# Kernel optimization log

Hardware: AMD Instinct MI355X
Metric: run time of the kernel (lower is better)

## Reference

```python
import jax, jax.numpy as jnp
import numpy as np

B, L, H, NH = 4, 200, 256, 4
HS = H // NH
NEG = jnp.float32(-(2.0**32) + 1.0)


def setup_inputs() -> dict:
    key = jax.random.key(0)
    ks = jax.random.split(key, 12)
    f = lambda k, s, sc=1.0: jax.random.normal(k, s, dtype=jnp.float32) * sc
    w_sc = 1.0 / np.sqrt(H).astype(np.float32)
    return {
        "queries": f(ks[0], (B, L, H)),
        "keys": f(ks[1], (B, L, H)),
        "time_matrix_K": f(ks[2], (B, L, L, H)),
        "time_matrix_V": f(ks[3], (B, L, L, H)),
        "dis_matrix_K": f(ks[4], (B, L, L, H)),
        "dis_matrix_V": f(ks[5], (B, L, L, H)),
        "abs_pos_K": f(ks[6], (B, L, H)),
        "abs_pos_V": f(ks[7], (B, L, H)),
        "Qw": f(ks[8], (H, H), w_sc),
        "Qb": jnp.zeros((H,), jnp.float32),
        "Kw": f(ks[9], (H, H), w_sc),
        "Kb": jnp.zeros((H,), jnp.float32),
        "Vw": f(ks[10], (H, H), w_sc),
        "Vb": jnp.zeros((H,), jnp.float32),
        "time_mask": jnp.zeros((B, L), dtype=bool),          # no padding positions
        "attn_mask": ~jnp.tril(jnp.ones((L, L), dtype=bool)),  # causal: mask strict upper triangle
    }


def reference(queries, keys, time_matrix_K, time_matrix_V, dis_matrix_K, dis_matrix_V,
              abs_pos_K, abs_pos_V, Qw, Qb, Kw, Kb, Vw, Vb, time_mask, attn_mask):
    # Linear projections (torch nn.Linear: x @ W^T + b)
    Q = queries @ Qw.T + Qb
    K = keys @ Kw.T + Kb
    V = keys @ Vw.T + Vb
    # split heads: [B, L, NH, HS]
    qh = Q.reshape(B, L, NH, HS)
    kh = K.reshape(B, L, NH, HS)
    vh = V.reshape(B, L, NH, HS)
    pKh = abs_pos_K.reshape(B, L, NH, HS)
    pVh = abs_pos_V.reshape(B, L, NH, HS)
    tKh = time_matrix_K.reshape(B, L, L, NH, HS)
    tVh = time_matrix_V.reshape(B, L, L, NH, HS)
    dKh = dis_matrix_K.reshape(B, L, L, NH, HS)
    dVh = dis_matrix_V.reshape(B, L, L, NH, HS)

    # attention logits [B, NH, L(query), L(key)] with three extra bias terms
    w = jnp.einsum("blhd,bmhd->bhlm", qh, kh)
    w += jnp.einsum("blhd,bmhd->bhlm", qh, pKh)
    w += jnp.einsum("blmhd,blhd->bhlm", tKh, qh)
    w += jnp.einsum("blmhd,blhd->bhlm", dKh, qh)
    w = w / jnp.sqrt(jnp.float32(HS))

    mask = time_mask[:, None, :, None] | attn_mask[None, None, :, :]
    w = jnp.where(mask, NEG, w)
    a = jax.nn.softmax(w, axis=-1)  # dropout_rate = 0 (eval)

    out = jnp.einsum("bhlm,bmhd->blhd", a, vh)
    out += jnp.einsum("bhlm,bmhd->blhd", a, pVh)
    out += jnp.einsum("bhlm,blmhd->blhd", a, tVh)
    out += jnp.einsum("bhlm,blmhd->blhd", a, dVh)
    return out.reshape(B, L, H)
```

## Files before the change

kernel.cpp:

```cpp
#include <hip/hip_runtime.h>
#include <cstddef>


#define B 4
#define L 200
#define H 256
#define NH 4
#define HS 64
#define SCALE 0.125f
#define NROWS 4

__global__ __launch_bounds__(256) void depoi_proj(
    const float* __restrict__ queries, const float* __restrict__ keys,
    const float* __restrict__ Qw, const float* __restrict__ Qb,
    const float* __restrict__ Kw, const float* __restrict__ Kb,
    const float* __restrict__ Vw, const float* __restrict__ Vb,
    const float* __restrict__ apK, const float* __restrict__ apV,
    float* __restrict__ Qo, float* __restrict__ Ko, float* __restrict__ Vo)
{
    __shared__ float4 xq[NROWS][H / 4];
    __shared__ float4 xk[NROWS][H / 4];
    const int t  = threadIdx.x;
    const int n0 = blockIdx.x * NROWS;

    const float4* q4 = (const float4*)queries;
    const float4* k4 = (const float4*)keys;
    {
        int r = t >> 6, c = t & 63;
        xq[r][c] = q4[(size_t)(n0 + r) * (H / 4) + c];
        xk[r][c] = k4[(size_t)(n0 + r) * (H / 4) + c];
    }
    __syncthreads();

    float accq[NROWS], acck[NROWS], accv[NROWS];
#pragma unroll
    for (int r = 0; r < NROWS; ++r) { accq[r] = 0.f; acck[r] = 0.f; accv[r] = 0.f; }

    const float4* Qw4 = (const float4*)Qw + (size_t)t * (H / 4);
    const float4* Kw4 = (const float4*)Kw + (size_t)t * (H / 4);
    const float4* Vw4 = (const float4*)Vw + (size_t)t * (H / 4);
    for (int i = 0; i < H / 4; ++i) {
        float4 wq = Qw4[i], wk = Kw4[i], wv = Vw4[i];
#pragma unroll
        for (int r = 0; r < NROWS; ++r) {
            float4 a = xq[r][i];
            float4 c = xk[r][i];
            accq[r] += a.x * wq.x + a.y * wq.y + a.z * wq.z + a.w * wq.w;
            acck[r] += c.x * wk.x + c.y * wk.y + c.z * wk.z + c.w * wk.w;
            accv[r] += c.x * wv.x + c.y * wv.y + c.z * wv.z + c.w * wv.w;
        }
    }

    const float bq = Qb[t], bk = Kb[t], bv = Vb[t];
#pragma unroll
    for (int r = 0; r < NROWS; ++r) {
        size_t o = (size_t)(n0 + r) * H + t;
        Qo[o] = accq[r] + bq;
        Ko[o] = acck[r] + bk + apK[o];
        Vo[o] = accv[r] + bv + apV[o];
    }
}

__global__ __launch_bounds__(512) void depoi_attn(
    const float* __restrict__ Q, const float* __restrict__ Ksum,
    const float* __restrict__ Vsum,
    const float* __restrict__ tK, const float* __restrict__ dK,
    const float* __restrict__ tV, const float* __restrict__ dV,
    float* __restrict__ out)
{
    const int l = L - 1 - blockIdx.x;
    const int b = blockIdx.y;
    const int t    = threadIdx.x;
    const int c    = t & 63;
    const int mg   = t >> 6;
    const int lane = t & 63;
    const int hh   = c >> 4;
    const int M    = l + 1;

    __shared__ float plog[NH][208];
    __shared__ float sredA[8];
    __shared__ float sredB[8];
    __shared__ float4 wpart[8][64];

    const float4* Q4 = (const float4*)Q;
    const float4 q4  = Q4[(size_t)(b * L + l) * 64 + c];

    const float4* K4 = (const float4*)Ksum + (size_t)b * L * 64;
    const float4* T4 = (const float4*)tK + (size_t)(b * L + l) * L * 64;
    const float4* D4 = (const float4*)dK + (size_t)(b * L + l) * L * 64;

    int m = mg;
    for (; m + 8 < M; m += 16) {
        float4 k0 = K4[(size_t)m * 64 + c];
        float4 t0 = T4[(size_t)m * 64 + c];
        float4 d0 = D4[(size_t)m * 64 + c];
        float4 k1 = K4[(size_t)(m + 8) * 64 + c];
        float4 t1 = T4[(size_t)(m + 8) * 64 + c];
        float4 d1 = D4[(size_t)(m + 8) * 64 + c];
        float p0 = q4.x * (k0.x + t0.x + d0.x) + q4.y * (k0.y + t0.y + d0.y)
                 + q4.z * (k0.z + t0.z + d0.z) + q4.w * (k0.w + t0.w + d0.w);
        float p1 = q4.x * (k1.x + t1.x + d1.x) + q4.y * (k1.y + t1.y + d1.y)
                 + q4.z * (k1.z + t1.z + d1.z) + q4.w * (k1.w + t1.w + d1.w);
        p0 += __shfl_xor(p0, 1); p1 += __shfl_xor(p1, 1);
        p0 += __shfl_xor(p0, 2); p1 += __shfl_xor(p1, 2);
        p0 += __shfl_xor(p0, 4); p1 += __shfl_xor(p1, 4);
        p0 += __shfl_xor(p0, 8); p1 += __shfl_xor(p1, 8);
        if ((c & 15) == 0) {
            plog[hh][m]     = p0 * SCALE;
            plog[hh][m + 8] = p1 * SCALE;
        }
    }
    if (m < M) {
        float4 k0 = K4[(size_t)m * 64 + c];
        float4 t0 = T4[(size_t)m * 64 + c];
        float4 d0 = D4[(size_t)m * 64 + c];
        float p0 = q4.x * (k0.x + t0.x + d0.x) + q4.y * (k0.y + t0.y + d0.y)
                 + q4.z * (k0.z + t0.z + d0.z) + q4.w * (k0.w + t0.w + d0.w);
        p0 += __shfl_xor(p0, 1);
        p0 += __shfl_xor(p0, 2);
        p0 += __shfl_xor(p0, 4);
        p0 += __shfl_xor(p0, 8);
        if ((c & 15) == 0) plog[hh][m] = p0 * SCALE;
    }
    __syncthreads();

    const int head = t >> 7;
    const int th   = t & 127;
    const int wid  = t >> 6;
    float x0 = (th < M)       ? plog[head][th]       : -3.0e38f;
    float x1 = (th + 128 < M) ? plog[head][th + 128] : -3.0e38f;
    float mx = fmaxf(x0, x1);
#pragma unroll
    for (int off = 32; off >= 1; off >>= 1) mx = fmaxf(mx, __shfl_xor(mx, off));
    if (lane == 0) sredA[wid] = mx;
    __syncthreads();
    mx = fmaxf(sredA[2 * head], sredA[2 * head + 1]);
    float e0 = (th < M)       ? __expf(x0 - mx) : 0.0f;
    float e1 = (th + 128 < M) ? __expf(x1 - mx) : 0.0f;
    if (th < M)       plog[head][th]       = e0;
    if (th + 128 < M) plog[head][th + 128] = e1;
    float s = e0 + e1;
#pragma unroll
    for (int off = 32; off >= 1; off >>= 1) s += __shfl_xor(s, off);
    if (lane == 0) sredB[wid] = s;
    __syncthreads();

    const float4* V4  = (const float4*)Vsum + (size_t)b * L * 64;
    const float4* TV4 = (const float4*)tV + (size_t)(b * L + l) * L * 64;
    const float4* DV4 = (const float4*)dV + (size_t)(b * L + l) * L * 64;
    float4 acc = make_float4(0.f, 0.f, 0.f, 0.f);
    m = mg;
    for (; m + 8 < M; m += 16) {
        float4 v0  = V4[(size_t)m * 64 + c];
        float4 tv0 = TV4[(size_t)m * 64 + c];
        float4 dv0 = DV4[(size_t)m * 64 + c];
        float4 v1  = V4[(size_t)(m + 8) * 64 + c];
        float4 tv1 = TV4[(size_t)(m + 8) * 64 + c];
        float4 dv1 = DV4[(size_t)(m + 8) * 64 + c];
        float pm0 = plog[hh][m];
        float pm1 = plog[hh][m + 8];
        acc.x += pm0 * (v0.x + tv0.x + dv0.x) + pm1 * (v1.x + tv1.x + dv1.x);
        acc.y += pm0 * (v0.y + tv0.y + dv0.y) + pm1 * (v1.y + tv1.y + dv1.y);
        acc.z += pm0 * (v0.z + tv0.z + dv0.z) + pm1 * (v1.z + tv1.z + dv1.z);
        acc.w += pm0 * (v0.w + tv0.w + dv0.w) + pm1 * (v1.w + tv1.w + dv1.w);
    }
    if (m < M) {
        float4 v0  = V4[(size_t)m * 64 + c];
        float4 tv0 = TV4[(size_t)m * 64 + c];
        float4 dv0 = DV4[(size_t)m * 64 + c];
        float pm0 = plog[hh][m];
        acc.x += pm0 * (v0.x + tv0.x + dv0.x);
        acc.y += pm0 * (v0.y + tv0.y + dv0.y);
        acc.z += pm0 * (v0.z + tv0.z + dv0.z);
        acc.w += pm0 * (v0.w + tv0.w + dv0.w);
    }
    wpart[mg][c] = acc;
    __syncthreads();

    if (t < 64) {
        float4 r = make_float4(0.f, 0.f, 0.f, 0.f);
#pragma unroll
        for (int i = 0; i < 8; ++i) {
            float4 w = wpart[i][t];
            r.x += w.x; r.y += w.y; r.z += w.z; r.w += w.w;
        }
        const float inv = 1.0f / (sredB[2 * (t >> 4)] + sredB[2 * (t >> 4) + 1]);
        r.x *= inv; r.y *= inv; r.z *= inv; r.w *= inv;
        ((float4*)out)[(size_t)(b * L + l) * 64 + t] = r;
    }
}

extern "C" void kernel_launch(void* const* d_in, const int* in_sizes, int n_in,
                              void* d_out, int out_size, void* d_ws, size_t ws_size,
                              hipStream_t stream) {
    const float* queries = (const float*)d_in[0];
    const float* keys    = (const float*)d_in[1];
    const float* tK      = (const float*)d_in[2];
    const float* tV      = (const float*)d_in[3];
    const float* dK      = (const float*)d_in[4];
    const float* dV      = (const float*)d_in[5];
    const float* apK     = (const float*)d_in[6];
    const float* apV     = (const float*)d_in[7];
    const float* Qw      = (const float*)d_in[8];
    const float* Qb      = (const float*)d_in[9];
    const float* Kw      = (const float*)d_in[10];
    const float* Kb      = (const float*)d_in[11];
    const float* Vw      = (const float*)d_in[12];
    const float* Vb      = (const float*)d_in[13];

    float* ws = (float*)d_ws;
    float* Qo = ws;
    float* Ko = ws + (size_t)B * L * H;
    float* Vo = ws + (size_t)2 * B * L * H;

    depoi_proj<<<(B * L) / NROWS, 256, 0, stream>>>(
        queries, keys, Qw, Qb, Kw, Kb, Vw, Vb, apK, apV, Qo, Ko, Vo);

    dim3 grid(L, B);
    depoi_attn<<<grid, 512, 0, stream>>>(Qo, Ko, Vo, tK, dK, tV, dV, (float*)d_out);
}
```

Baseline: 533.0 us.

## Fuse logit and value passes with online softmax in attention kernel

```diff
diff --git a/kernel.cpp b/kernel.cpp
--- a/kernel.cpp
+++ b/kernel.cpp
@@ -61,42 +61,49 @@
     }
 }
 
-__global__ __launch_bounds__(512) void depoi_attn(
+__global__ __launch_bounds__(512, 4) void depoi_attn(
     const float* __restrict__ Q, const float* __restrict__ Ksum,
     const float* __restrict__ Vsum,
     const float* __restrict__ tK, const float* __restrict__ dK,
     const float* __restrict__ tV, const float* __restrict__ dV,
     float* __restrict__ out)
 {
-    const int l = L - 1 - blockIdx.x;
-    const int b = blockIdx.y;
-    const int t    = threadIdx.x;
-    const int c    = t & 63;
-    const int mg   = t >> 6;
-    const int lane = t & 63;
-    const int hh   = c >> 4;
-    const int M    = l + 1;
-
-    __shared__ float plog[NH][208];
-    __shared__ float sredA[8];
-    __shared__ float sredB[8];
-    __shared__ float4 wpart[8][64];
-
-    const float4* Q4 = (const float4*)Q;
-    const float4 q4  = Q4[(size_t)(b * L + l) * 64 + c];
-
-    const float4* K4 = (const float4*)Ksum + (size_t)b * L * 64;
-    const float4* T4 = (const float4*)tK + (size_t)(b * L + l) * L * 64;
-    const float4* D4 = (const float4*)dK + (size_t)(b * L + l) * L * 64;
+    const int l  = L - 1 - blockIdx.x;
+    const int b  = blockIdx.y;
+    const int t  = threadIdx.x;
+    const int c  = t & 63;
+    const int mg = t >> 6;
+    const int M  = l + 1;
+
+    __shared__ float4 wacc[8][64];
+    __shared__ float  wmax[8][NH];
+    __shared__ float  wsum[8][NH];
+
+    float4 q4 = ((const float4*)Q)[(size_t)(b * L + l) * 64 + c];
+    q4.x *= SCALE; q4.y *= SCALE; q4.z *= SCALE; q4.w *= SCALE;
+
+    const float4* K4  = (const float4*)Ksum + (size_t)b * L * 64 + c;
+    const float4* V4  = (const float4*)Vsum + (size_t)b * L * 64 + c;
+    const float4* T4  = (const float4*)tK + (size_t)(b * L + l) * L * 64 + c;
+    const float4* D4  = (const float4*)dK + (size_t)(b * L + l) * L * 64 + c;
+    const float4* TV4 = (const float4*)tV + (size_t)(b * L + l) * L * 64 + c;
+    const float4* DV4 = (const float4*)dV + (size_t)(b * L + l) * L * 64 + c;
+
+    float4 acc   = make_float4(0.f, 0.f, 0.f, 0.f);
+    float  run_m = -3.0e38f;
+    float  run_s = 0.f;
 
     int m = mg;
     for (; m + 8 < M; m += 16) {
-        float4 k0 = K4[(size_t)m * 64 + c];
-        float4 t0 = T4[(size_t)m * 64 + c];
-        float4 d0 = D4[(size_t)m * 64 + c];
-        float4 k1 = K4[(size_t)(m + 8) * 64 + c];
-        float4 t1 = T4[(size_t)(m + 8) * 64 + c];
-        float4 d1 = D4[(size_t)(m + 8) * 64 + c];
+        const size_t o0 = (size_t)m * 64;
+        const size_t o1 = (size_t)(m + 8) * 64;
+        float4 k0  = K4[o0],  k1  = K4[o1];
+        float4 t0  = T4[o0],  t1  = T4[o1];
+        float4 d0  = D4[o0],  d1  = D4[o1];
+        float4 v0  = V4[o0],  v1  = V4[o1];
+        float4 tv0 = TV4[o0], tv1 = TV4[o1];
+        float4 dv0 = DV4[o0], dv1 = DV4[o1];
+
         float p0 = q4.x * (k0.x + t0.x + d0.x) + q4.y * (k0.y + t0.y + d0.y)
                  + q4.z * (k0.z + t0.z + d0.z) + q4.w * (k0.w + t0.w + d0.w);
         float p1 = q4.x * (k1.x + t1.x + d1.x) + q4.y * (k1.y + t1.y + d1.y)
@@ -105,86 +112,65 @@
         p0 += __shfl_xor(p0, 2); p1 += __shfl_xor(p1, 2);
         p0 += __shfl_xor(p0, 4); p1 += __shfl_xor(p1, 4);
         p0 += __shfl_xor(p0, 8); p1 += __shfl_xor(p1, 8);
-        if ((c & 15) == 0) {
-            plog[hh][m]     = p0 * SCALE;
-            plog[hh][m + 8] = p1 * SCALE;
-        }
+
+        float nm = fmaxf(run_m, fmaxf(p0, p1));
+        float sc = __expf(run_m - nm);
+        float e0 = __expf(p0 - nm);
+        float e1 = __expf(p1 - nm);
+        run_m = nm;
+        run_s = run_s * sc + e0 + e1;
+        acc.x = acc.x * sc + e0 * (v0.x + tv0.x + dv0.x) + e1 * (v1.x + tv1.x + dv1.x);
+        acc.y = acc.y * sc + e0 * (v0.y + tv0.y + dv0.y) + e1 * (v1.y + tv1.y + dv1.y);
+        acc.z = acc.z * sc + e0 * (v0.z + tv0.z + dv0.z) + e1 * (v1.z + tv1.z + dv1.z);
+        acc.w = acc.w * sc + e0 * (v0.w + tv0.w + dv0.w) + e1 * (v1.w + tv1.w + dv1.w);
     }
     if (m < M) {
-        float4 k0 = K4[(size_t)m * 64 + c];
-        float4 t0 = T4[(size_t)m * 64 + c];
-        float4 d0 = D4[(size_t)m * 64 + c];
+        const size_t o0 = (size_t)m * 64;
+        float4 k0  = K4[o0];
+        float4 t0  = T4[o0];
+        float4 d0  = D4[o0];
+        float4 v0  = V4[o0];
+        float4 tv0 = TV4[o0];
+        float4 dv0 = DV4[o0];
         float p0 = q4.x * (k0.x + t0.x + d0.x) + q4.y * (k0.y + t0.y + d0.y)
                  + q4.z * (k0.z + t0.z + d0.z) + q4.w * (k0.w + t0.w + d0.w);
         p0 += __shfl_xor(p0, 1);
         p0 += __shfl_xor(p0, 2);
         p0 += __shfl_xor(p0, 4);
         p0 += __shfl_xor(p0, 8);
-        if ((c & 15) == 0) plog[hh][m] = p0 * SCALE;
+        float nm = fmaxf(run_m, p0);
+        float sc = __expf(run_m - nm);
+        float e0 = __expf(p0 - nm);
+        run_m = nm;
+        run_s = run_s * sc + e0;
+        acc.x = acc.x * sc + e0 * (v0.x + tv0.x + dv0.x);
+        acc.y = acc.y * sc + e0 * (v0.y + tv0.y + dv0.y);
+        acc.z = acc.z * sc + e0 * (v0.z + tv0.z + dv0.z);
+        acc.w = acc.w * sc + e0 * (v0.w + tv0.w + dv0.w);
+    }
+
+    wacc[mg][c] = acc;
+    if ((c & 15) == 0) {
+        wmax[mg][c >> 4] = run_m;
+        wsum[mg][c >> 4] = run_s;
     }
     __syncthreads();
 
-    const int head = t >> 7;
-    const int th   = t & 127;
-    const int wid  = t >> 6;
-    float x0 = (th < M)       ? plog[head][th]       : -3.0e38f;
-    float x1 = (th + 128 < M) ? plog[head][th + 128] : -3.0e38f;
-    float mx = fmaxf(x0, x1);
-#pragma unroll
-    for (int off = 32; off >= 1; off >>= 1) mx = fmaxf(mx, __shfl_xor(mx, off));
-    if (lane == 0) sredA[wid] = mx;
-    __syncthreads();
-    mx = fmaxf(sredA[2 * head], sredA[2 * head + 1]);
-    float e0 = (th < M)       ? __expf(x0 - mx) : 0.0f;
-    float e1 = (th + 128 < M) ? __expf(x1 - mx) : 0.0f;
-    if (th < M)       plog[head][th]       = e0;
-    if (th + 128 < M) plog[head][th + 128] = e1;
-    float s = e0 + e1;
-#pragma unroll
-    for (int off = 32; off >= 1; off >>= 1) s += __shfl_xor(s, off);
-    if (lane == 0) sredB[wid] = s;
-    __syncthreads();
-
-    const float4* V4  = (const float4*)Vsum + (size_t)b * L * 64;
-    const float4* TV4 = (const float4*)tV + (size_t)(b * L + l) * L * 64;
-    const float4* DV4 = (const float4*)dV + (size_t)(b * L + l) * L * 64;
-    float4 acc = make_float4(0.f, 0.f, 0.f, 0.f);
-    m = mg;
-    for (; m + 8 < M; m += 16) {
-        float4 v0  = V4[(size_t)m * 64 + c];
-        float4 tv0 = TV4[(size_t)m * 64 + c];
-        float4 dv0 = DV4[(size_t)m * 64 + c];
-        float4 v1  = V4[(size_t)(m + 8) * 64 + c];
-        float4 tv1 = TV4[(size_t)(m + 8) * 64 + c];
-        float4 dv1 = DV4[(size_t)(m + 8) * 64 + c];
-        float pm0 = plog[hh][m];
-        float pm1 = plog[hh][m + 8];
-        acc.x += pm0 * (v0.x + tv0.x + dv0.x) + pm1 * (v1.x + tv1.x + dv1.x);
-        acc.y += pm0 * (v0.y + tv0.y + dv0.y) + pm1 * (v1.y + tv1.y + dv1.y);
-        acc.z += pm0 * (v0.z + tv0.z + dv0.z) + pm1 * (v1.z + tv1.z + dv1.z);
-        acc.w += pm0 * (v0.w + tv0.w + dv0.w) + pm1 * (v1.w + tv1.w + dv1.w);
-    }
-    if (m < M) {
-        float4 v0  = V4[(size_t)m * 64 + c];
-        float4 tv0 = TV4[(size_t)m * 64 + c];
-        float4 dv0 = DV4[(size_t)m * 64 + c];
-        float pm0 = plog[hh][m];
-        acc.x += pm0 * (v0.x + tv0.x + dv0.x);
-        acc.y += pm0 * (v0.y + tv0.y + dv0.y);
-        acc.z += pm0 * (v0.z + tv0.z + dv0.z);
-        acc.w += pm0 * (v0.w + tv0.w + dv0.w);
-    }
-    wpart[mg][c] = acc;
-    __syncthreads();
-
     if (t < 64) {
+        const int h = t >> 4;
+        float gm = wmax[0][h];
+#pragma unroll
+        for (int i = 1; i < 8; ++i) gm = fmaxf(gm, wmax[i][h]);
         float4 r = make_float4(0.f, 0.f, 0.f, 0.f);
+        float  s = 0.f;
 #pragma unroll
         for (int i = 0; i < 8; ++i) {
-            float4 w = wpart[i][t];
-            r.x += w.x; r.y += w.y; r.z += w.z; r.w += w.w;
+            float sc = __expf(wmax[i][h] - gm);
+            float4 w = wacc[i][t];
+            r.x += sc * w.x; r.y += sc * w.y; r.z += sc * w.z; r.w += sc * w.w;
+            s += sc * wsum[i][h];
         }
-        const float inv = 1.0f / (sredB[2 * (t >> 4)] + sredB[2 * (t >> 4) + 1]);
+        const float inv = 1.0f / s;
         r.x *= inv; r.y *= inv; r.z *= inv; r.w *= inv;
         ((float4*)out)[(size_t)(b * L + l) * 64 + t] = r;
     }
```

Result: no change. 536.5 us (+0.6%).
